# Kernel optimization log

Measured on AMD Instinct MI355X. Metric: run time of the kernel, lower is better.

Reference implementation:

```python
import jax, jax.numpy as jnp
import numpy as np

N_NODES = 384
HEIGHT = 60
LN_EPS = 1e-5


def setup_inputs() -> dict:
    key = jax.random.key(0)
    ks = jax.random.split(key, 6)
    C = 256
    E = 3072
    x = jax.random.normal(ks[0], (N_NODES, C, HEIGHT), dtype=jnp.float32)
    edge_attr = jax.random.normal(ks[1], (E, 5), dtype=jnp.float32)
    edge_index = jax.random.randint(ks[2], (2, E), 0, N_NODES)
    W_edge = jax.random.normal(ks[3], (5, C), dtype=jnp.float32) * 0.3
    b_edge = jnp.zeros((C,), dtype=jnp.float32)
    W_conv = jax.random.normal(ks[4], (C, 3 * C), dtype=jnp.float32) * (1.0 / np.sqrt(3 * C))
    ln_gamma = jnp.ones((C, HEIGHT), dtype=jnp.float32)
    ln_beta = jnp.zeros((C, HEIGHT), dtype=jnp.float32)
    return {"x": x, "edge_attr": edge_attr, "edge_index": edge_index,
            "W_edge": W_edge, "b_edge": b_edge, "W_conv": W_conv,
            "ln_gamma": ln_gamma, "ln_beta": ln_beta}


def reference(x, edge_attr, edge_index, W_edge, b_edge, W_conv, ln_gamma, ln_beta):
    # x: (N, C, 60); PyG convention: edge_index[0]=source (j), edge_index[1]=target (i)
    C = x.shape[1]
    src, dst = edge_index[0], edge_index[1]
    h_i = x[dst]                    # (E, C, 60) gather target features
    h_j = x[src]                    # (E, C, 60) gather source features
    ea = edge_attr @ W_edge + b_edge            # (E, C) edge Linear
    ea = jnp.broadcast_to(ea[:, :, None], h_i.shape)  # repeat over height
    h = jnp.concatenate([h_i, h_j - h_i, ea], axis=1)  # (E, 3C, 60)
    # Conv1d kernel_size=1, bias=False -> channel contraction
    m = jnp.einsum('ech,oc->eoh', h, W_conv)    # (E, C, 60)
    # LayerNorm over (C, 60) per edge
    mu = jnp.mean(m, axis=(1, 2), keepdims=True)
    var = jnp.var(m, axis=(1, 2), keepdims=True)
    m = (m - mu) * jax.lax.rsqrt(var + LN_EPS) * ln_gamma + ln_beta
    m = jax.nn.relu(m)
    # aggr='add' scatter into target nodes
    out = jax.ops.segment_sum(m.reshape(m.shape[0], C * HEIGHT), dst,
                              num_segments=N_NODES)
    return out.reshape(N_NODES, C, HEIGHT)
```

## Files before the change

kernel.cpp:

```cpp
#include <hip/hip_runtime.h>

#define N_NODES 384
#define CCH 256
#define HT 60
#define CH (CCH*HT)
#define CH4 (CH/4)
#define LN_EPS 1e-5f
#define KSPLIT 40

typedef __attribute__((ext_vector_type(8))) short bf16x8;
typedef __attribute__((ext_vector_type(4))) float f32x4;

__device__ inline unsigned short f2bf(float f) {
    unsigned int u = __float_as_uint(f);
    unsigned int r = (u + 0x7FFF + ((u >> 16) & 1)) >> 16;
    return (unsigned short)r;
}
__device__ inline float bf2f(unsigned short u) {
    return __uint_as_float(((unsigned int)u) << 16);
}

__global__ __launch_bounds__(1024) void k_setup(const float* __restrict__ Wc,
                                                unsigned short* __restrict__ Wfrag) {
    int idx = blockIdx.x * 1024 + threadIdx.x;
    int j = idx & 7, lane = (idx >> 3) & 63, ks = (idx >> 9) & 7, mt = idx >> 12;
    int o = mt * 16 + (lane & 15);
    int c = ks * 32 + (lane >> 4) * 8 + j;
    float v;
    if (o < 256) v = Wc[o * 768 + c] - Wc[o * 768 + 256 + c];
    else         v = Wc[(o - 256) * 768 + 256 + c];
    Wfrag[idx] = f2bf(v);
}

__global__ __launch_bounds__(256) void k_node_mfma(const float* __restrict__ x,
                                                   const unsigned short* __restrict__ Wfrag,
                                                   unsigned short* __restrict__ Abf,
                                                   unsigned short* __restrict__ Bbf) {
    __shared__ unsigned short xT[32 * 256];
    int n = blockIdx.x, half = blockIdx.y, tid = threadIdx.x;

    const float4* xg = (const float4*)(x + (size_t)n * CH);
    if (half == 0) {
        for (int i = tid; i < 2048; i += 256) {
            int c = i >> 3, jj = i & 7;
            int r0 = jj * 4;
            float4 v = xg[c * 15 + jj];
            xT[(r0+0) * 256 + (c ^ (((r0+0) & 7) << 3))] = f2bf(v.x);
            xT[(r0+1) * 256 + (c ^ (((r0+1) & 7) << 3))] = f2bf(v.y);
            xT[(r0+2) * 256 + (c ^ (((r0+2) & 7) << 3))] = f2bf(v.z);
            xT[(r0+3) * 256 + (c ^ (((r0+3) & 7) << 3))] = f2bf(v.w);
        }
    } else {
        for (int i = tid; i < 4 * 256; i += 256) {
            int r = 28 + (i >> 8), c = i & 255;
            xT[r * 256 + (c ^ ((r & 7) << 3))] = 0;
        }
        for (int i = tid; i < 1792; i += 256) {
            int c = i / 7, jj = i - c * 7;
            int r0 = jj * 4;
            float4 v = xg[c * 15 + 8 + jj];
            xT[(r0+0) * 256 + (c ^ (((r0+0) & 7) << 3))] = f2bf(v.x);
            xT[(r0+1) * 256 + (c ^ (((r0+1) & 7) << 3))] = f2bf(v.y);
            xT[(r0+2) * 256 + (c ^ (((r0+2) & 7) << 3))] = f2bf(v.z);
            xT[(r0+3) * 256 + (c ^ (((r0+3) & 7) << 3))] = f2bf(v.w);
        }
    }
    __syncthreads();

    int w = tid >> 6, lane = tid & 63;
    int l15 = lane & 15, lg = lane >> 4;

    f32x4 acc[8][2];
#pragma unroll
    for (int mt = 0; mt < 8; ++mt)
#pragma unroll
        for (int nt = 0; nt < 2; ++nt)
            acc[mt][nt] = (f32x4){0.f, 0.f, 0.f, 0.f};

    const unsigned short* wbase = Wfrag + ((size_t)(w * 8) * 8) * 64 * 8;
    for (int ks = 0; ks < 8; ++ks) {
        bf16x8 bfr[2];
#pragma unroll
        for (int nt = 0; nt < 2; ++nt) {
            int row = nt * 16 + l15;
            int col = ks * 32 + lg * 8;
            int idx = row * 256 + (col ^ ((row & 7) << 3));
            bfr[nt] = *(const bf16x8*)(&xT[idx]);
        }
#pragma unroll
        for (int mt = 0; mt < 8; ++mt) {
            const bf16x8 afr = *(const bf16x8*)(wbase + (((size_t)mt * 8 + ks) * 64 + lane) * 8);
#pragma unroll
            for (int nt = 0; nt < 2; ++nt)
                acc[mt][nt] = __builtin_amdgcn_mfma_f32_16x16x32_bf16(afr, bfr[nt], acc[mt][nt], 0, 0, 0);
        }
    }

#pragma unroll
    for (int mt = 0; mt < 8; ++mt) {
        int mtg = w * 8 + mt;
        int obase = mtg * 16 + 4 * lg;
        unsigned short* dst0 = (obase < 256)
            ? (Abf + (size_t)n * CH + (size_t)obase * 60)
            : (Bbf + (size_t)n * CH + (size_t)(obase - 256) * 60);
#pragma unroll
        for (int nt = 0; nt < 2; ++nt) {
            int h = half * 32 + nt * 16 + l15;
            if (h < 60) {
#pragma unroll
                for (int r = 0; r < 4; ++r)
                    dst0[r * 60 + h] = f2bf(acc[mt][nt][r]);
            }
        }
    }
}

__global__ __launch_bounds__(256) void k_gramscal(const unsigned short* __restrict__ Abf,
                                                  const unsigned short* __restrict__ Bbf,
                                                  const float* __restrict__ Wc,
                                                  const float* __restrict__ We,
                                                  const float* __restrict__ be,
                                                  const int* __restrict__ dst, int E,
                                                  float* __restrict__ Gpart,
                                                  float* __restrict__ RAB,
                                                  float4* __restrict__ Sc,
                                                  float* __restrict__ M,
                                                  float* __restrict__ bias0,
                                                  int* __restrict__ offs,
                                                  int* __restrict__ elist) {
    int b = blockIdx.x;
    int tid = threadIdx.x, w = tid >> 6, lane = tid & 63;
    int l15 = lane & 15, lg = lane >> 4;
    if (b == 0) {
        __shared__ int cnt[N_NODES];
        __shared__ int sc0[N_NODES], sc1[N_NODES];
        for (int i = tid; i < N_NODES; i += 256) cnt[i] = 0;
        __syncthreads();
        for (int e = tid; e < E; e += 256) atomicAdd(&cnt[dst[e]], 1);
        __syncthreads();
        for (int i = tid; i < N_NODES; i += 256) sc0[i] = cnt[i];
        __syncthreads();
        int flip = 0;
        for (int d = 1; d < N_NODES; d <<= 1) {
            const int* s_ = flip ? sc1 : sc0;
            int* d_ = flip ? sc0 : sc1;
            for (int i = tid; i < N_NODES; i += 256)
                d_[i] = s_[i] + (i >= d ? s_[i - d] : 0);
            __syncthreads();
            flip ^= 1;
        }
        const int* pos = flip ? sc1 : sc0;
        for (int i = tid; i < N_NODES; i += 256) {
            offs[i + 1] = pos[i];
            cnt[i] = (i == 0) ? 0 : pos[i - 1];
        }
        if (tid == 0) offs[0] = 0;
        __syncthreads();
        for (int e = tid; e < E; e += 256) {
            int d = dst[e];
            elist[atomicAdd(&cnt[d], 1)] = e;
        }
        __syncthreads();
        for (int n2 = tid; n2 < N_NODES; n2 += 256) {
            int lo = (n2 == 0) ? 0 : pos[n2 - 1], hi = pos[n2];
            for (int i = lo + 1; i < hi; ++i) {
                int key = elist[i]; int j = i - 1;
                while (j >= lo && elist[j] > key) { elist[j + 1] = elist[j]; --j; }
                elist[j + 1] = key;
            }
        }
        return;
    }
    if (b == 1) {
        int o = tid;
        float m0=0,m1=0,m2=0,m3=0,m4=0,bb=0;
        for (int k = 0; k < 256; ++k) {
            float w3 = Wc[o * 768 + 512 + k];
            m0 += We[0*256+k] * w3;
            m1 += We[1*256+k] * w3;
            m2 += We[2*256+k] * w3;
            m3 += We[3*256+k] * w3;
            m4 += We[4*256+k] * w3;
            bb += be[k] * w3;
        }
        M[0*256+o]=m0; M[1*256+o]=m1; M[2*256+o]=m2; M[3*256+o]=m3; M[4*256+o]=m4;
        bias0[o] = bb;
        return;
    }
    if (b < 362) {
        int g = b - 2;
        int ks = g / 9, rem = g - ks * 9, bi = rem % 3, bj = rem / 3;
        int d0 = bi * 128 + (w & 1) * 64;
        int s0 = bj * 128 + (w >> 1) * 64;
        int ksbase = ks * 384 + lg * 8;

        const unsigned short* Ap[4];
        const unsigned short* Bp[4];
#pragma unroll
        for (int t = 0; t < 4; ++t) {
            Ap[t] = Abf + (size_t)(d0 + t * 16 + l15) * CH + ksbase;
            Bp[t] = Bbf + (size_t)(s0 + t * 16 + l15) * CH + ksbase;
        }

        f32x4 acc[4][4];
#pragma unroll
        for (int a = 0; a < 4; ++a)
#pragma unroll
            for (int bb = 0; bb < 4; ++bb) acc[a][bb] = (f32x4){0.f,0.f,0.f,0.f};

        bf16x8 a0[4], b0[4], a1[4], b1[4];
#pragma unroll
        for (int t = 0; t < 4; ++t) {
            a0[t] = *(const bf16x8*)(Ap[t]);
            b0[t] = *(const bf16x8*)(Bp[t]);
        }
#pragma unroll
        for (int kk = 0; kk < 12; kk += 2) {
            if (kk + 1 < 12) {
#pragma unroll
                for (int t = 0; t < 4; ++t) {
                    a1[t] = *(const bf16x8*)(Ap[t] + (kk + 1) * 32);
                    b1[t] = *(const bf16x8*)(Bp[t] + (kk + 1) * 32);
                }
            }
#pragma unroll
            for (int a = 0; a < 4; ++a)
#pragma unroll
                for (int bb = 0; bb < 4; ++bb)
                    acc[a][bb] = __builtin_amdgcn_mfma_f32_16x16x32_bf16(a0[a], b0[bb], acc[a][bb], 0, 0, 0);
            if (kk + 2 < 12) {
#pragma unroll
                for (int t = 0; t < 4; ++t) {
                    a0[t] = *(const bf16x8*)(Ap[t] + (kk + 2) * 32);
                    b0[t] = *(const bf16x8*)(Bp[t] + (kk + 2) * 32);
                }
            }
#pragma unroll
            for (int a = 0; a < 4; ++a)
#pragma unroll
                for (int bb = 0; bb < 4; ++bb)
                    acc[a][bb] = __builtin_amdgcn_mfma_f32_16x16x32_bf16(a1[a], b1[bb], acc[a][bb], 0, 0, 0);
        }

        float* gp = Gpart + (size_t)ks * 384 * 384;
#pragma unroll
        for (int a = 0; a < 4; ++a)
#pragma unroll
            for (int bb = 0; bb < 4; ++bb) {
                int d = d0 + a * 16 + 4 * lg;
                int s = s0 + bb * 16 + l15;
#pragma unroll
                for (int r = 0; r < 4; ++r)
                    gp[(size_t)(d + r) * 384 + s] = acc[a][bb][r];
            }
    } else {
        __shared__ float red[16];
        int n = b - 362;
        const ushort4* Ab = (const ushort4*)(Abf + (size_t)n * CH + tid * 60);
        const ushort4* Bb = (const ushort4*)(Bbf + (size_t)n * CH + tid * 60);
        float rsA = 0.f, qA = 0.f, rsB = 0.f, qB = 0.f;
#pragma unroll
        for (int i = 0; i < 15; ++i) {
            ushort4 a = Ab[i], bb2 = Bb[i];
#pragma unroll
            for (int j = 0; j < 4; ++j) {
                float va = bf2f(((const unsigned short*)&a)[j]);
                float vb = bf2f(((const unsigned short*)&bb2)[j]);
                rsA += va; qA += va * va;
                rsB += vb; qB += vb * vb;
            }
        }
        RAB[(size_t)n * 512 + tid] = rsA;
        RAB[(size_t)n * 512 + 256 + tid] = rsB;
        float sA = rsA, sB = rsB;
#pragma unroll
        for (int o = 32; o >= 1; o >>= 1) {
            sA += __shfl_xor(sA, o, 64); qA += __shfl_xor(qA, o, 64);
            sB += __shfl_xor(sB, o, 64); qB += __shfl_xor(qB, o, 64);
        }
        if (lane == 0) { red[w*4]=sA; red[w*4+1]=qA; red[w*4+2]=sB; red[w*4+3]=qB; }
        __syncthreads();
        if (tid == 0) {
            Sc[n] = make_float4(red[0]+red[4]+red[8]+red[12],
                                red[1]+red[5]+red[9]+red[13],
                                red[2]+red[6]+red[10]+red[14],
                                red[3]+red[7]+red[11]+red[15]);
        }
    }
}

__global__ __launch_bounds__(256) void k_stats2(const float* __restrict__ ea,
                                                const float* __restrict__ M,
                                                const float* __restrict__ bias0,
                                                const int* __restrict__ srcA,
                                                const int* __restrict__ dstA, int E,
                                                const float* __restrict__ RAB,
                                                const float4* __restrict__ Sc,
                                                const float* __restrict__ Gpart,
                                                float* __restrict__ cbuf,
                                                float2* __restrict__ stats) {
    int w = threadIdx.x >> 6, lane = threadIdx.x & 63;
    int e = blockIdx.x * 4 + w;
    if (e >= E) return;
    int s = srcA[e], d = dstA[e];
    float ev0 = ea[e*5], ev1 = ea[e*5+1], ev2 = ea[e*5+2], ev3 = ea[e*5+3], ev4 = ea[e*5+4];
    float sc = 0.f, sc2 = 0.f, dots = 0.f;
#pragma unroll
    for (int r = 0; r < 4; ++r) {
        int o = lane + 64 * r;
        float c = bias0[o] + ev0*M[o] + ev1*M[256+o] + ev2*M[512+o] + ev3*M[768+o] + ev4*M[1024+o];
        cbuf[(size_t)e * 256 + o] = c;
        sc += c; sc2 += c * c;
        dots += (RAB[(size_t)d * 512 + o] + RAB[(size_t)s * 512 + 256 + o]) * c;
    }
    float g = (lane < KSPLIT) ? Gpart[((size_t)lane * 384 + d) * 384 + s] : 0.f;
#pragma unroll
    for (int o2 = 32; o2 >= 1; o2 >>= 1) {
        sc   += __shfl_xor(sc, o2, 64);
        sc2  += __shfl_xor(sc2, o2, 64);
        dots += __shfl_xor(dots, o2, 64);
        g    += __shfl_xor(g, o2, 64);
    }
    if (lane == 0) {
        float4 scd = Sc[d], scs = Sc[s];
        float S1 = scd.x + scs.z + 60.f * sc;
        float S2 = scd.y + scs.w + 60.f * sc2 + 2.f * (g + dots);
        float mu = S1 * (1.0f / (float)CH);
        float var = S2 * (1.0f / (float)CH) - mu * mu;
        stats[e] = make_float2(mu, rsqrtf(var + LN_EPS));
    }
}

__global__ __launch_bounds__(256) void k_apply(const unsigned short* __restrict__ Abf,
                                               const unsigned short* __restrict__ Bbf,
                                               const float* __restrict__ cbuf,
                                               const float2* __restrict__ stats,
                                               const int* __restrict__ srcArr,
                                               const int* __restrict__ offsets,
                                               const int* __restrict__ elist,
                                               const float* __restrict__ gamma,
                                               const float* __restrict__ beta,
                                               float* __restrict__ out) {
    int b = blockIdx.x;
    int cg8 = b & 7;
    int n = b >> 3;
    int tid = threadIdx.x;
    size_t sbase = (size_t)n * CH + (size_t)cg8 * 1920;
    const ushort4* Ab = (const ushort4*)(Abf + sbase);
    const float4*  g4 = (const float4*)(gamma + (size_t)cg8 * 1920);
    const float4*  b4 = (const float4*)(beta  + (size_t)cg8 * 1920);
    bool act1 = (tid < 224);

    float4 af[2], gv[2], bv[2], acc[2];
    int ci[2];
#pragma unroll
    for (int r = 0; r < 2; ++r) {
        acc[r] = make_float4(0.f, 0.f, 0.f, 0.f);
        af[r] = make_float4(0.f, 0.f, 0.f, 0.f);
        gv[r] = make_float4(0.f, 0.f, 0.f, 0.f);
        bv[r] = make_float4(0.f, 0.f, 0.f, 0.f);
        ci[r] = 0;
    }
#pragma unroll
    for (int r = 0; r < 2; ++r) {
        if (r == 0 || act1) {
            int i = tid + 256 * r;
            ci[r] = i / 15;
            ushort4 aw = Ab[i];
            af[r].x = bf2f(aw.x); af[r].y = bf2f(aw.y);
            af[r].z = bf2f(aw.z); af[r].w = bf2f(aw.w);
            gv[r] = g4[i];
            bv[r] = b4[i];
        }
    }

    int lo = offsets[n], hi = offsets[n + 1];
    int k = lo;
    for (; k + 1 < hi; k += 2) {
        int e0 = elist[k], e1 = elist[k + 1];
        int s0 = srcArr[e0], s1 = srcArr[e1];
        float2 st0 = stats[e0], st1 = stats[e1];
        const ushort4* B0 = (const ushort4*)(Bbf + (size_t)s0 * CH + (size_t)cg8 * 1920);
        const ushort4* B1 = (const ushort4*)(Bbf + (size_t)s1 * CH + (size_t)cg8 * 1920);
        const float* c0 = cbuf + (size_t)e0 * 256 + cg8 * 32;
        const float* c1 = cbuf + (size_t)e1 * 256 + cg8 * 32;
#pragma unroll
        for (int r = 0; r < 2; ++r) {
            if (r == 0 || act1) {
                int i = tid + 256 * r;
                ushort4 bw0 = B0[i];
                ushort4 bw1 = B1[i];
                float cc0 = c0[ci[r]];
                float cc1 = c1[ci[r]];
                float m0x = af[r].x + bf2f(bw0.x) + cc0;
                float m0y = af[r].y + bf2f(bw0.y) + cc0;
                float m0z = af[r].z + bf2f(bw0.z) + cc0;
                float m0w = af[r].w + bf2f(bw0.w) + cc0;
                float m1x = af[r].x + bf2f(bw1.x) + cc1;
                float m1y = af[r].y + bf2f(bw1.y) + cc1;
                float m1z = af[r].z + bf2f(bw1.z) + cc1;
                float m1w = af[r].w + bf2f(bw1.w) + cc1;
                acc[r].x += fmaxf((m0x - st0.x) * st0.y * gv[r].x + bv[r].x, 0.f);
                acc[r].y += fmaxf((m0y - st0.x) * st0.y * gv[r].y + bv[r].y, 0.f);
                acc[r].z += fmaxf((m0z - st0.x) * st0.y * gv[r].z + bv[r].z, 0.f);
                acc[r].w += fmaxf((m0w - st0.x) * st0.y * gv[r].w + bv[r].w, 0.f);
                acc[r].x += fmaxf((m1x - st1.x) * st1.y * gv[r].x + bv[r].x, 0.f);
                acc[r].y += fmaxf((m1y - st1.x) * st1.y * gv[r].y + bv[r].y, 0.f);
                acc[r].z += fmaxf((m1z - st1.x) * st1.y * gv[r].z + bv[r].z, 0.f);
                acc[r].w += fmaxf((m1w - st1.x) * st1.y * gv[r].w + bv[r].w, 0.f);
            }
        }
    }
    if (k < hi) {
        int e = elist[k];
        int s = srcArr[e];
        float2 st = stats[e];
        const ushort4* Bb = (const ushort4*)(Bbf + (size_t)s * CH + (size_t)cg8 * 1920);
        const float* cc = cbuf + (size_t)e * 256 + cg8 * 32;
#pragma unroll
        for (int r = 0; r < 2; ++r) {
            if (r == 0 || act1) {
                int i = tid + 256 * r;
                float ccv = cc[ci[r]];
                ushort4 bw = Bb[i];
                float mx = af[r].x + bf2f(bw.x) + ccv;
                float my = af[r].y + bf2f(bw.y) + ccv;
                float mz = af[r].z + bf2f(bw.z) + ccv;
                float mw = af[r].w + bf2f(bw.w) + ccv;
                acc[r].x += fmaxf((mx - st.x) * st.y * gv[r].x + bv[r].x, 0.f);
                acc[r].y += fmaxf((my - st.x) * st.y * gv[r].y + bv[r].y, 0.f);
                acc[r].z += fmaxf((mz - st.x) * st.y * gv[r].z + bv[r].z, 0.f);
                acc[r].w += fmaxf((mw - st.x) * st.y * gv[r].w + bv[r].w, 0.f);
            }
        }
    }
    float4* ob = (float4*)(out + sbase);
#pragma unroll
    for (int r = 0; r < 2; ++r)
        if (r == 0 || act1) ob[tid + 256 * r] = acc[r];
}

extern "C" void kernel_launch(void* const* d_in, const int* in_sizes, int n_in,
                              void* d_out, int out_size, void* d_ws, size_t ws_size,
                              hipStream_t stream) {
    const float* x     = (const float*)d_in[0];
    const float* ea    = (const float*)d_in[1];
    const int*   ei    = (const int*)d_in[2];
    const float* We    = (const float*)d_in[3];
    const float* be    = (const float*)d_in[4];
    const float* Wc    = (const float*)d_in[5];
    const float* gamma = (const float*)d_in[6];
    const float* beta  = (const float*)d_in[7];
    const int E = in_sizes[2] / 2;
    const int* src = ei;
    const int* dst = ei + E;

    char* ws = (char*)d_ws;
    size_t off = 0;
    auto alloc = [&](size_t bytes) -> void* {
        void* p = ws + off;
        off += (bytes + 255) & ~(size_t)255;
        return p;
    };
    unsigned short* Abf    = (unsigned short*)alloc((size_t)N_NODES * CH * 2);
    unsigned short* Bbf    = (unsigned short*)alloc((size_t)N_NODES * CH * 2);
    float*          cbuf   = (float*)alloc((size_t)E * 256 * 4);
    float2*         stats  = (float2*)alloc((size_t)E * 8);
    unsigned short* Wfrag  = (unsigned short*)alloc(512 * 256 * 2);
    float*          M      = (float*)alloc(5 * 256 * 4);
    float*          bias0  = (float*)alloc(256 * 4);
    float*          RAB    = (float*)alloc((size_t)N_NODES * 512 * 4);
    float4*         Sc     = (float4*)alloc((size_t)N_NODES * 16);
    float*          Gpart  = (float*)alloc((size_t)KSPLIT * 384 * 384 * 4);
    int*            offs   = (int*)alloc((N_NODES + 1) * 4);
    int*            elist  = (int*)alloc((size_t)E * 4);

    k_setup<<<128, 1024, 0, stream>>>(Wc, Wfrag);
    k_node_mfma<<<dim3(N_NODES, 2), 256, 0, stream>>>(x, Wfrag, Abf, Bbf);
    k_gramscal<<<746, 256, 0, stream>>>(Abf, Bbf, Wc, We, be, dst, E,
                                        Gpart, RAB, Sc, M, bias0, offs, elist);
    k_stats2<<<(E + 3) / 4, 256, 0, stream>>>(ea, M, bias0, src, dst, E, RAB, Sc, Gpart,
                                              cbuf, stats);
    k_apply<<<N_NODES * 8, 256, 0, stream>>>(Abf, Bbf, cbuf, stats, src, offs, elist,
                                             gamma, beta, (float*)d_out);
}
```

Measured before the change: 89.11 us.

## Replace full node Gram matrix with per-edge direct A·B dot products

Drops the split-K MFMA Gram computation over all 384x384 node pairs, along with its partial-sum buffer. Each edge block now computes the dot product of A[dst] and B[src] directly from the bf16 node features and reduces it in shared memory. This avoids computing node pairs that no edge uses and avoids writing and rereading the large partial buffer. In exchange, each edge rereads two 15360-element rows, about 3072 edges times 61 KB of traffic, which is largely served from L2. It also switches the stats kernel from one wave per edge to one block per edge.

```diff
diff --git a/kernel.cpp b/kernel.cpp
--- a/kernel.cpp
+++ b/kernel.cpp
@@ -6,7 +6,6 @@
 #define CH (CCH*HT)
 #define CH4 (CH/4)
 #define LN_EPS 1e-5f
-#define KSPLIT 40
 
 typedef __attribute__((ext_vector_type(8))) short bf16x8;
 typedef __attribute__((ext_vector_type(4))) float f32x4;
@@ -115,13 +114,12 @@
     }
 }
 
-__global__ __launch_bounds__(256) void k_gramscal(const unsigned short* __restrict__ Abf,
+__global__ __launch_bounds__(256) void k_prepscal(const unsigned short* __restrict__ Abf,
                                                   const unsigned short* __restrict__ Bbf,
                                                   const float* __restrict__ Wc,
                                                   const float* __restrict__ We,
                                                   const float* __restrict__ be,
                                                   const int* __restrict__ dst, int E,
-                                                  float* __restrict__ Gpart,
                                                   float* __restrict__ RAB,
                                                   float4* __restrict__ Sc,
                                                   float* __restrict__ M,
@@ -130,7 +128,6 @@
                                                   int* __restrict__ elist) {
     int b = blockIdx.x;
     int tid = threadIdx.x, w = tid >> 6, lane = tid & 63;
-    int l15 = lane & 15, lg = lane >> 4;
     if (b == 0) {
         __shared__ int cnt[N_NODES];
         __shared__ int sc0[N_NODES], sc1[N_NODES];
@@ -187,75 +184,9 @@
         bias0[o] = bb;
         return;
     }
-    if (b < 362) {
-        int g = b - 2;
-        int ks = g / 9, rem = g - ks * 9, bi = rem % 3, bj = rem / 3;
-        int d0 = bi * 128 + (w & 1) * 64;
-        int s0 = bj * 128 + (w >> 1) * 64;
-        int ksbase = ks * 384 + lg * 8;
-
-        const unsigned short* Ap[4];
-        const unsigned short* Bp[4];
-#pragma unroll
-        for (int t = 0; t < 4; ++t) {
-            Ap[t] = Abf + (size_t)(d0 + t * 16 + l15) * CH + ksbase;
-            Bp[t] = Bbf + (size_t)(s0 + t * 16 + l15) * CH + ksbase;
-        }
-
-        f32x4 acc[4][4];
-#pragma unroll
-        for (int a = 0; a < 4; ++a)
-#pragma unroll
-            for (int bb = 0; bb < 4; ++bb) acc[a][bb] = (f32x4){0.f,0.f,0.f,0.f};
-
-        bf16x8 a0[4], b0[4], a1[4], b1[4];
-#pragma unroll
-        for (int t = 0; t < 4; ++t) {
-            a0[t] = *(const bf16x8*)(Ap[t]);
-            b0[t] = *(const bf16x8*)(Bp[t]);
-        }
-#pragma unroll
-        for (int kk = 0; kk < 12; kk += 2) {
-            if (kk + 1 < 12) {
-#pragma unroll
-                for (int t = 0; t < 4; ++t) {
-                    a1[t] = *(const bf16x8*)(Ap[t] + (kk + 1) * 32);
-                    b1[t] = *(const bf16x8*)(Bp[t] + (kk + 1) * 32);
-                }
-            }
-#pragma unroll
-            for (int a = 0; a < 4; ++a)
-#pragma unroll
-                for (int bb = 0; bb < 4; ++bb)
-                    acc[a][bb] = __builtin_amdgcn_mfma_f32_16x16x32_bf16(a0[a], b0[bb], acc[a][bb], 0, 0, 0);
-            if (kk + 2 < 12) {
-#pragma unroll
-                for (int t = 0; t < 4; ++t) {
-                    a0[t] = *(const bf16x8*)(Ap[t] + (kk + 2) * 32);
-                    b0[t] = *(const bf16x8*)(Bp[t] + (kk + 2) * 32);
-                }
-            }
-#pragma unroll
-            for (int a = 0; a < 4; ++a)
-#pragma unroll
-                for (int bb = 0; bb < 4; ++bb)
-                    acc[a][bb] = __builtin_amdgcn_mfma_f32_16x16x32_bf16(a1[a], b1[bb], acc[a][bb], 0, 0, 0);
-        }
-
-        float* gp = Gpart + (size_t)ks * 384 * 384;
-#pragma unroll
-        for (int a = 0; a < 4; ++a)
-#pragma unroll
-            for (int bb = 0; bb < 4; ++bb) {
-                int d = d0 + a * 16 + 4 * lg;
-                int s = s0 + bb * 16 + l15;
-#pragma unroll
-                for (int r = 0; r < 4; ++r)
-                    gp[(size_t)(d + r) * 384 + s] = acc[a][bb][r];
-            }
-    } else {
+    {
         __shared__ float red[16];
-        int n = b - 362;
+        int n = b - 2;
         const ushort4* Ab = (const ushort4*)(Abf + (size_t)n * CH + tid * 60);
         const ushort4* Bb = (const ushort4*)(Bbf + (size_t)n * CH + tid * 60);
         float rsA = 0.f, qA = 0.f, rsB = 0.f, qB = 0.f;
@@ -289,42 +220,57 @@
     }
 }
 
-__global__ __launch_bounds__(256) void k_stats2(const float* __restrict__ ea,
+__global__ __launch_bounds__(256) void k_estats(const unsigned short* __restrict__ Abf,
+                                                const unsigned short* __restrict__ Bbf,
+                                                const float* __restrict__ ea,
                                                 const float* __restrict__ M,
                                                 const float* __restrict__ bias0,
                                                 const int* __restrict__ srcA,
-                                                const int* __restrict__ dstA, int E,
+                                                const int* __restrict__ dstA,
                                                 const float* __restrict__ RAB,
                                                 const float4* __restrict__ Sc,
-                                                const float* __restrict__ Gpart,
                                                 float* __restrict__ cbuf,
                                                 float2* __restrict__ stats) {
-    int w = threadIdx.x >> 6, lane = threadIdx.x & 63;
-    int e = blockIdx.x * 4 + w;
-    if (e >= E) return;
+    __shared__ float red[16];
+    int e = blockIdx.x;
+    int tid = threadIdx.x, w = tid >> 6, lane = tid & 63;
     int s = srcA[e], d = dstA[e];
+
     float ev0 = ea[e*5], ev1 = ea[e*5+1], ev2 = ea[e*5+2], ev3 = ea[e*5+3], ev4 = ea[e*5+4];
-    float sc = 0.f, sc2 = 0.f, dots = 0.f;
-#pragma unroll
-    for (int r = 0; r < 4; ++r) {
-        int o = lane + 64 * r;
-        float c = bias0[o] + ev0*M[o] + ev1*M[256+o] + ev2*M[512+o] + ev3*M[768+o] + ev4*M[1024+o];
-        cbuf[(size_t)e * 256 + o] = c;
-        sc += c; sc2 += c * c;
-        dots += (RAB[(size_t)d * 512 + o] + RAB[(size_t)s * 512 + 256 + o]) * c;
-    }
-    float g = (lane < KSPLIT) ? Gpart[((size_t)lane * 384 + d) * 384 + s] : 0.f;
+    int o = tid;
+    float c = bias0[o] + ev0*M[o] + ev1*M[256+o] + ev2*M[512+o] + ev3*M[768+o] + ev4*M[1024+o];
+    cbuf[(size_t)e * 256 + o] = c;
+    float sc = c, sc2 = c * c;
+    float dots = (RAB[(size_t)d * 512 + o] + RAB[(size_t)s * 512 + 256 + o]) * c;
+
+    const ushort4* Ab = (const ushort4*)(Abf + (size_t)d * CH);
+    const ushort4* Bb = (const ushort4*)(Bbf + (size_t)s * CH);
+    float dot = 0.f;
+#pragma unroll
+    for (int r = 0; r < 15; ++r) {
+        ushort4 a = Ab[tid + 256 * r];
+        ushort4 b = Bb[tid + 256 * r];
+        dot += bf2f(a.x) * bf2f(b.x) + bf2f(a.y) * bf2f(b.y)
+             + bf2f(a.z) * bf2f(b.z) + bf2f(a.w) * bf2f(b.w);
+    }
+
 #pragma unroll
     for (int o2 = 32; o2 >= 1; o2 >>= 1) {
         sc   += __shfl_xor(sc, o2, 64);
         sc2  += __shfl_xor(sc2, o2, 64);
         dots += __shfl_xor(dots, o2, 64);
-        g    += __shfl_xor(g, o2, 64);
-    }
-    if (lane == 0) {
+        dot  += __shfl_xor(dot, o2, 64);
+    }
+    if (lane == 0) { red[w*4]=sc; red[w*4+1]=sc2; red[w*4+2]=dots; red[w*4+3]=dot; }
+    __syncthreads();
+    if (tid == 0) {
+        float S_c   = red[0] + red[4] + red[8]  + red[12];
+        float S_c2  = red[1] + red[5] + red[9]  + red[13];
+        float S_dts = red[2] + red[6] + red[10] + red[14];
+        float S_dot = red[3] + red[7] + red[11] + red[15];
         float4 scd = Sc[d], scs = Sc[s];
-        float S1 = scd.x + scs.z + 60.f * sc;
-        float S2 = scd.y + scs.w + 60.f * sc2 + 2.f * (g + dots);
+        float S1 = scd.x + scs.z + 60.f * S_c;
+        float S2 = scd.y + scs.w + 60.f * S_c2 + 2.f * (S_dot + S_dts);
         float mu = S1 * (1.0f / (float)CH);
         float var = S2 * (1.0f / (float)CH) - mu * mu;
         stats[e] = make_float2(mu, rsqrtf(var + LN_EPS));
@@ -471,16 +417,15 @@
     float*          bias0  = (float*)alloc(256 * 4);
     float*          RAB    = (float*)alloc((size_t)N_NODES * 512 * 4);
     float4*         Sc     = (float4*)alloc((size_t)N_NODES * 16);
-    float*          Gpart  = (float*)alloc((size_t)KSPLIT * 384 * 384 * 4);
     int*            offs   = (int*)alloc((N_NODES + 1) * 4);
     int*            elist  = (int*)alloc((size_t)E * 4);
 
     k_setup<<<128, 1024, 0, stream>>>(Wc, Wfrag);
     k_node_mfma<<<dim3(N_NODES, 2), 256, 0, stream>>>(x, Wfrag, Abf, Bbf);
-    k_gramscal<<<746, 256, 0, stream>>>(Abf, Bbf, Wc, We, be, dst, E,
-                                        Gpart, RAB, Sc, M, bias0, offs, elist);
-    k_stats2<<<(E + 3) / 4, 256, 0, stream>>>(ea, M, bias0, src, dst, E, RAB, Sc, Gpart,
-                                              cbuf, stats);
+    k_prepscal<<<2 + N_NODES, 256, 0, stream>>>(Abf, Bbf, Wc, We, be, dst, E,
+                                                RAB, Sc, M, bias0, offs, elist);
+    k_estats<<<E, 256, 0, stream>>>(Abf, Bbf, ea, M, bias0, src, dst, RAB, Sc,
+                                    cbuf, stats);
     k_apply<<<N_NODES * 8, 256, 0, stream>>>(Abf, Bbf, cbuf, stats, src, offs, elist,
                                              gamma, beta, (float*)d_out);
 }
```

Result: slower. 99.43 us (+11.6%).
